# Kernel tuning notes

Hardware: AMD Instinct MI355X
Metric: run time of the kernel (lower is better)

Reference implementation:

```python
import jax, jax.numpy as jnp
import numpy as np

V, E, H, L, B, T = 8192, 64, 256, 2, 4, 512


def setup_inputs() -> dict:
    key = jax.random.key(0)
    ks = jax.random.split(key, 20)
    s = 0.02
    emb = (jax.random.normal(ks[0], (V, E)) * s).at[0].set(0.0)  # padding_idx=0
    x = jax.random.randint(ks[1], (B, T), 0, V)
    return {
        "x": x,
        "emb": emb,
        "W_ih0": jax.random.normal(ks[2], (H, E)) * s,
        "W_hh0": jax.random.normal(ks[3], (H, H)) * s,
        "b_ih0": jnp.zeros((H,), jnp.float32),
        "b_hh0": jnp.zeros((H,), jnp.float32),
        "W_ih1": jax.random.normal(ks[4], (H, H)) * s,
        "W_hh1": jax.random.normal(ks[5], (H, H)) * s,
        "b_ih1": jnp.zeros((H,), jnp.float32),
        "b_hh1": jnp.zeros((H,), jnp.float32),
        "Wq": jax.random.normal(ks[6], (H, H)) * s,
        "Wk": jax.random.normal(ks[7], (H, H)) * s,
        "v": jax.random.normal(ks[8], (H,)) * s,
        "gamma": jnp.ones((2 * H,), jnp.float32),
        "beta": jnp.zeros((2 * H,), jnp.float32),
        "Wfc": jax.random.normal(ks[9], (V, 2 * H)) * s,
        "bfc": jnp.zeros((V,), jnp.float32),
    }


def _rnn_layer(xs, W_ih, W_hh, b_ih, b_hh):
    # xs: (B, T, D) -> ys: (B, T, H), hT: (B, H). Vanilla tanh RNN.
    Bn = xs.shape[0]
    Hn = W_hh.shape[0]
    h0 = jnp.zeros((Bn, Hn), xs.dtype)

    def step(h, xt):
        h_new = jnp.tanh(xt @ W_ih.T + b_ih + h @ W_hh.T + b_hh)
        return h_new, h_new

    hT, ys = jax.lax.scan(step, h0, jnp.swapaxes(xs, 0, 1))
    return jnp.swapaxes(ys, 0, 1), hT


def reference(x, emb, W_ih0, W_hh0, b_ih0, b_hh0, W_ih1, W_hh1, b_ih1, b_hh1,
              Wq, Wk, v, gamma, beta, Wfc, bfc):
    # Dropout layers are identity (eval mode).
    e = emb[x]                                   # (B, T, E)
    y0, h0 = _rnn_layer(e, W_ih0, W_hh0, b_ih0, b_hh0)
    y1, h1 = _rnn_layer(y0, W_ih1, W_hh1, b_ih1, b_hh1)  # (B, T, H)

    # Bahdanau additive attention with causal mask
    q = y1 @ Wq.T                                # (B, T, H)
    k = y1 @ Wk.T                                # (B, T, H)
    # (B, Tq, Tk, H) broadcast add -> tanh -> contract with v
    scores = jnp.einsum('bijh,h->bij', jnp.tanh(q[:, :, None, :] + k[:, None, :, :]), v)
    Tn = scores.shape[1]
    causal = jnp.tril(jnp.ones((Tn, Tn), bool))
    scores = jnp.where(causal[None], scores, jnp.float32(-1e9))
    alpha = jax.nn.softmax(scores, axis=-1)      # (B, Tq, Tk)
    ctx = jnp.einsum('bij,bjh->bih', alpha, y1)  # bmm(alpha, K) with K = rnn_out

    cat = jnp.concatenate([y1, ctx], axis=-1)    # (B, T, 2H)
    mu = cat.mean(-1, keepdims=True)
    var = ((cat - mu) ** 2).mean(-1, keepdims=True)
    normed = (cat - mu) / jnp.sqrt(var + 1e-5) * gamma + beta

    logits = normed @ Wfc.T + bfc                # (B, T, V)
    h = jnp.stack([h0, h1], axis=0)              # (L, B, H)
    return logits, h
```

## Files before the change

kernel.cpp:

```cpp
#include <hip/hip_runtime.h>
#include <hip/hip_bf16.h>

typedef __bf16 bf16x8 __attribute__((ext_vector_type(8)));
typedef float  f32x4  __attribute__((ext_vector_type(4)));
typedef unsigned short u16;

#define T_N 512
#define H_N 256
#define B_N 4
#define V_N 8192
#define E_N 64

__device__ __forceinline__ float tanh_fast(float x) {
    float e = __expf(2.0f * x);
    return 1.0f - __fdividef(2.0f, e + 1.0f);
}

__device__ __forceinline__ u16 f2bf(float f) {
    __hip_bfloat16 h = __float2bfloat16(f);
    return __builtin_bit_cast(u16, h);
}

__device__ __forceinline__ bf16x8 as_bf16x8(uint4 u) {
    return __builtin_bit_cast(bf16x8, u);
}

__device__ __forceinline__ uint4 pack_bf8(f32x4 lo, f32x4 hi) {
    union { u16 s[8]; uint4 u; } r;
    #pragma unroll
    for (int e = 0; e < 4; ++e) { r.s[e] = f2bf(lo[e]); r.s[e+4] = f2bf(hi[e]); }
    return r.u;
}

__device__ __forceinline__ f32x4 mfma16(bf16x8 a, bf16x8 b, f32x4 c) {
    return __builtin_amdgcn_mfma_f32_16x16x32_bf16(a, b, c, 0, 0, 0);
}

__global__ void cvt_bf16_kernel(const float* __restrict__ src, u16* __restrict__ dst, int n4) {
    int i = blockIdx.x * 256 + threadIdx.x;
    if (i < n4) {
        f32x4 v = ((const f32x4*)src)[i];
        union { u16 s[4]; unsigned long long u; } r;
        #pragma unroll
        for (int e = 0; e < 4; ++e) r.s[e] = f2bf(v[e]);
        ((unsigned long long*)dst)[i] = r.u;
    }
}

__global__ __launch_bounds__(256)
void embed_xw0_kernel(const int* __restrict__ x, const float* __restrict__ emb,
                      const float* __restrict__ Wih, const float* __restrict__ bih,
                      const float* __restrict__ bhh, float* __restrict__ xw0) {
    const int t = blockIdx.x, tid = threadIdx.x;
    __shared__ float sE[4][64];
    {
        const int b = tid >> 6, k = tid & 63;
        sE[b][k] = emb[(size_t)x[b * T_N + t] * E_N + k];
    }
    __syncthreads();
    const int j = tid;
    const float* wr = Wih + j * E_N;
    float a0 = 0, a1 = 0, a2 = 0, a3 = 0;
    #pragma unroll 8
    for (int k = 0; k < E_N; ++k) {
        float wv = wr[k];
        a0 += sE[0][k] * wv; a1 += sE[1][k] * wv;
        a2 += sE[2][k] * wv; a3 += sE[3][k] * wv;
    }
    const float bs = bih[j] + bhh[j];
    f32x4 o = { a0 + bs, a1 + bs, a2 + bs, a3 + bs };
    *(f32x4*)(xw0 + ((size_t)t * H_N + j) * 4) = o;
}

template<int STORE_F32>
__global__ __launch_bounds__(256, 1)
void rnn_rec_kernel(const float* __restrict__ Whh, const float* __restrict__ xw,
                    u16* __restrict__ ybf, float* __restrict__ yf32,
                    float* __restrict__ hT) {
    __shared__ __align__(16) u16 hbuf[2][4][288];

    const int tid = threadIdx.x;
    const int w = tid >> 6, l = tid & 63;
    const int m = l & 15, g = l >> 4;
    const int b4 = m & 3;
    const int jmy = (w << 6) + l;

    for (int idx = tid; idx < 2 * 4 * 288; idx += 256) (&hbuf[0][0][0])[idx] = (u16)0;

    bf16x8 wfrag[4][8];
    #pragma unroll
    for (int nt = 0; nt < 4; ++nt) {
        const int j = (w << 6) + (nt << 4) + m;
        #pragma unroll
        for (int kk = 0; kk < 8; ++kk) {
            const float* p = Whh + (size_t)j * H_N + (kk << 5) + (g << 3);
            f32x4 lo = *(const f32x4*)p;
            f32x4 hi = *(const f32x4*)(p + 4);
            wfrag[nt][kk] = as_bf16x8(pack_bf8(lo, hi));
        }
    }

    const f32x4* xwv = (const f32x4*)xw;
    f32x4 xw_cur = xwv[jmy];
    __syncthreads();

    int cur = 0;
    for (int t = 0; t < T_N; ++t) {
        const int tn = (t + 1 < T_N) ? (t + 1) : t;
        f32x4 xw_nxt = xwv[(size_t)tn * H_N + jmy];

        bf16x8 af[8];
        #pragma unroll
        for (int kk = 0; kk < 8; ++kk)
            af[kk] = as_bf16x8(*(const uint4*)&hbuf[cur][b4][(kk << 5) + (g << 3)]);

        f32x4 ca[4], cb[4];
        #pragma unroll
        for (int nt = 0; nt < 4; ++nt) {
            ca[nt] = (f32x4){0.f, 0.f, 0.f, 0.f};
            cb[nt] = (f32x4){0.f, 0.f, 0.f, 0.f};
        }
        #pragma unroll
        for (int kk = 0; kk < 4; ++kk)
            #pragma unroll
            for (int nt = 0; nt < 4; ++nt) {
                ca[nt] = mfma16(af[kk],     wfrag[nt][kk],     ca[nt]);
                cb[nt] = mfma16(af[kk + 4], wfrag[nt][kk + 4], cb[nt]);
            }

        f32x4 hv = (g == 0) ? (ca[0] + cb[0])
                 : (g == 1) ? (ca[1] + cb[1])
                 : (g == 2) ? (ca[2] + cb[2])
                 :            (ca[3] + cb[3]);
        hv += xw_cur;

        #pragma unroll
        for (int b = 0; b < 4; ++b) {
            float hn = tanh_fast(hv[b]);
            u16 bits = f2bf(hn);
            hbuf[cur ^ 1][b][jmy] = bits;
            ybf[((size_t)b * T_N + t) * H_N + jmy] = bits;
            if (STORE_F32) yf32[((size_t)b * T_N + t) * H_N + jmy] = hn;
            if (t == T_N - 1) hT[b * H_N + jmy] = hn;
        }
        xw_cur = xw_nxt;
        cur ^= 1;

        asm volatile("s_waitcnt lgkmcnt(0)" ::: "memory");
        __builtin_amdgcn_s_barrier();
        __builtin_amdgcn_sched_barrier(0);
    }
}

template<int MODE>
__global__ __launch_bounds__(256, 2)
void gemm_bf16(const u16* __restrict__ A, const u16* __restrict__ Bw,
               float* __restrict__ out, const float* __restrict__ bias,
               const float* __restrict__ bias2, int M, int N, int K) {
    __shared__ __align__(16) u16 As[64][40];
    __shared__ __align__(16) u16 Bs[64][40];
    const int tid = threadIdx.x;
    const int nb = N >> 6;
    const int bm = blockIdx.x / nb, bn = blockIdx.x % nb;
    const int l = tid & 63, w = tid >> 6;
    const int wm = w & 1, wn = w >> 1;
    const int m = l & 15, g = l >> 4;
    const int srow = tid >> 2, sseg = tid & 3;

    f32x4 c[2][2];
    #pragma unroll
    for (int i = 0; i < 2; ++i)
        #pragma unroll
        for (int j = 0; j < 2; ++j) c[i][j] = (f32x4){0.f, 0.f, 0.f, 0.f};

    const u16* ap = A  + (size_t)(bm * 64 + srow) * K + sseg * 8;
    const u16* bp = Bw + (size_t)(bn * 64 + srow) * K + sseg * 8;

    for (int k0 = 0; k0 < K; k0 += 32) {
        uint4 av = *(const uint4*)(ap + k0);
        uint4 bv = *(const uint4*)(bp + k0);
        __syncthreads();
        *(uint4*)&As[srow][sseg << 3] = av;
        *(uint4*)&Bs[srow][sseg << 3] = bv;
        __syncthreads();
        bf16x8 af[2], bfr[2];
        #pragma unroll
        for (int i = 0; i < 2; ++i) {
            af[i]  = as_bf16x8(*(const uint4*)&As[(wm << 5) + (i << 4) + m][g << 3]);
            bfr[i] = as_bf16x8(*(const uint4*)&Bs[(wn << 5) + (i << 4) + m][g << 3]);
        }
        #pragma unroll
        for (int i = 0; i < 2; ++i)
            #pragma unroll
            for (int j = 0; j < 2; ++j)
                c[i][j] = mfma16(af[i], bfr[j], c[i][j]);
    }

    #pragma unroll
    for (int i = 0; i < 2; ++i)
        #pragma unroll
        for (int j = 0; j < 2; ++j) {
            const int col = (bn << 6) + (wn << 5) + (j << 4) + m;
            float bs = 0.f;
            if (bias)  bs += bias[col];
            if (bias2) bs += bias2[col];
            #pragma unroll
            for (int r = 0; r < 4; ++r) {
                const int row = (bm << 6) + (wm << 5) + (i << 4) + (g << 2) + r;
                const float val = c[i][j][r] + bs;
                if (MODE == 0) {
                    out[(size_t)row * N + col] = val;
                } else if (MODE == 1) {
                    const int b = row >> 9, t = row & 511;
                    out[((size_t)t * N + col) * 4 + b] = val;
                } else {
                    const int b = row >> 9, t = row & 511;
                    out[(size_t)b * N * T_N + (size_t)col * T_N + t] = val;
                }
            }
        }
}

__global__ __launch_bounds__(256, 2)
void gemm_fc(const u16* __restrict__ A, const u16* __restrict__ Bw,
             const float* __restrict__ bias, float* __restrict__ out) {
    __shared__ __align__(16) u16 As[128 * 32];
    __shared__ __align__(16) u16 Bs[128 * 32];
    const int tid = threadIdx.x;
    const int l = tid & 63, w = tid >> 6;
    const int m = l & 15, g = l >> 4;
    const int wm = w >> 1, wn = w & 1;
    const int bm = blockIdx.x >> 6, bn = blockIdx.x & 63;
    constexpr int K = 512;

    f32x4 acc[4][4];
    #pragma unroll
    for (int i = 0; i < 4; ++i)
        #pragma unroll
        for (int j = 0; j < 4; ++j) acc[i][j] = (f32x4){0.f, 0.f, 0.f, 0.f};

    const u16* aBase = A  + (size_t)(bm * 128) * K;
    const u16* bBase = Bw + (size_t)(bn * 128) * K;
    const int row0 = tid >> 2,          seg0 = tid & 3;
    const int row1 = (tid + 256) >> 2,  seg1 = tid & 3;
    const int wseg0 = seg0 ^ ((row0 >> 1) & 3);
    const int wseg1 = seg1 ^ ((row1 >> 1) & 3);

    for (int k0 = 0; k0 < K; k0 += 32) {
        uint4 av0 = *(const uint4*)(aBase + (size_t)row0 * K + k0 + seg0 * 8);
        uint4 av1 = *(const uint4*)(aBase + (size_t)row1 * K + k0 + seg1 * 8);
        uint4 bv0 = *(const uint4*)(bBase + (size_t)row0 * K + k0 + seg0 * 8);
        uint4 bv1 = *(const uint4*)(bBase + (size_t)row1 * K + k0 + seg1 * 8);
        __syncthreads();
        *(uint4*)((char*)As + row0 * 64 + wseg0 * 16) = av0;
        *(uint4*)((char*)As + row1 * 64 + wseg1 * 16) = av1;
        *(uint4*)((char*)Bs + row0 * 64 + wseg0 * 16) = bv0;
        *(uint4*)((char*)Bs + row1 * 64 + wseg1 * 16) = bv1;
        __syncthreads();
        bf16x8 af[4], bfr[4];
        #pragma unroll
        for (int i = 0; i < 4; ++i) {
            const int arow = wm * 64 + i * 16 + m;
            const int aslot = g ^ ((arow >> 1) & 3);
            af[i]  = as_bf16x8(*(const uint4*)((char*)As + arow * 64 + aslot * 16));
            const int brow = wn * 64 + i * 16 + m;
            const int bslot = g ^ ((brow >> 1) & 3);
            bfr[i] = as_bf16x8(*(const uint4*)((char*)Bs + brow * 64 + bslot * 16));
        }
        #pragma unroll
        for (int i = 0; i < 4; ++i)
            #pragma unroll
            for (int j = 0; j < 4; ++j)
                acc[i][j] = mfma16(af[i], bfr[j], acc[i][j]);
    }

    #pragma unroll
    for (int i = 0; i < 4; ++i)
        #pragma unroll
        for (int j = 0; j < 4; ++j) {
            const int col = bn * 128 + wn * 64 + j * 16 + m;
            const float bs = bias[col];
            #pragma unroll
            for (int r = 0; r < 4; ++r) {
                const int row = bm * 128 + wm * 64 + i * 16 + (g << 2) + r;
                out[(size_t)row * V_N + col] = acc[i][j][r] + bs;
            }
        }
}

__global__ __launch_bounds__(256)
void attn_kernel(const float* __restrict__ q, const float* __restrict__ kT,
                 const float* __restrict__ y1f, const float* __restrict__ vvec,
                 float* __restrict__ ctx) {
    const int blk = blockIdx.x;
    const int b = blk >> 9, i = blk & 511;
    const int tid = threadIdx.x;
    __shared__ float sQ[H_N], sV[H_N], sS[T_N];
    __shared__ float red[4];
    sQ[tid] = q[((size_t)b * T_N + i) * H_N + tid];
    sV[tid] = vvec[tid];
    __syncthreads();

    float s0 = -1e30f, s1 = -1e30f;
    if (tid <= i) {
        const float* kp = kT + (size_t)b * H_N * T_N + tid;
        float acc = 0.f;
        for (int h = 0; h < H_N; ++h) acc += sV[h] * tanh_fast(sQ[h] + kp[(size_t)h * T_N]);
        s0 = acc;
    }
    if (tid + 256 <= i) {
        const float* kp = kT + (size_t)b * H_N * T_N + tid + 256;
        float acc = 0.f;
        for (int h = 0; h < H_N; ++h) acc += sV[h] * tanh_fast(sQ[h] + kp[(size_t)h * T_N]);
        s1 = acc;
    }
    float mv = fmaxf(s0, s1);
    #pragma unroll
    for (int o = 32; o; o >>= 1) mv = fmaxf(mv, __shfl_xor(mv, o, 64));
    if ((tid & 63) == 0) red[tid >> 6] = mv;
    __syncthreads();
    mv = fmaxf(fmaxf(red[0], red[1]), fmaxf(red[2], red[3]));
    __syncthreads();
    float e0 = (tid <= i)       ? __expf(s0 - mv) : 0.f;
    float e1 = (tid + 256 <= i) ? __expf(s1 - mv) : 0.f;
    float sm = e0 + e1;
    #pragma unroll
    for (int o = 32; o; o >>= 1) sm += __shfl_xor(sm, o, 64);
    if ((tid & 63) == 0) red[tid >> 6] = sm;
    __syncthreads();
    sm = red[0] + red[1] + red[2] + red[3];
    const float rs = 1.0f / sm;
    sS[tid] = e0 * rs;
    sS[tid + 256] = e1 * rs;
    __syncthreads();
    float acc = 0.f;
    const float* yp = y1f + (size_t)b * T_N * H_N + tid;
    for (int j2 = 0; j2 <= i; ++j2) acc += sS[j2] * yp[(size_t)j2 * H_N];
    ctx[((size_t)b * T_N + i) * H_N + tid] = acc;
}

__global__ __launch_bounds__(256)
void ln_kernel(const float* __restrict__ y1f, const float* __restrict__ ctx,
               const float* __restrict__ gamma, const float* __restrict__ beta,
               u16* __restrict__ outbf) {
    const int row = blockIdx.x, tid = threadIdx.x;
    __shared__ float red[4];
    const float x1 = y1f[(size_t)row * H_N + tid];
    const float x2 = ctx[(size_t)row * H_N + tid];
    float s = x1 + x2;
    #pragma unroll
    for (int o = 32; o; o >>= 1) s += __shfl_xor(s, o, 64);
    if ((tid & 63) == 0) red[tid >> 6] = s;
    __syncthreads();
    const float mu = (red[0] + red[1] + red[2] + red[3]) * (1.f / 512.f);
    __syncthreads();
    const float d1 = x1 - mu, d2 = x2 - mu;
    float qv = d1 * d1 + d2 * d2;
    #pragma unroll
    for (int o = 32; o; o >>= 1) qv += __shfl_xor(qv, o, 64);
    if ((tid & 63) == 0) red[tid >> 6] = qv;
    __syncthreads();
    const float var = (red[0] + red[1] + red[2] + red[3]) * (1.f / 512.f);
    const float inv = rsqrtf(var + 1e-5f);
    outbf[(size_t)row * 512 + tid]       = f2bf(d1 * inv * gamma[tid] + beta[tid]);
    outbf[(size_t)row * 512 + tid + 256] = f2bf(d2 * inv * gamma[tid + 256] + beta[tid + 256]);
}

extern "C" void kernel_launch(void* const* d_in, const int* in_sizes, int n_in,
                              void* d_out, int out_size, void* d_ws, size_t ws_size,
                              hipStream_t stream) {
    const int*   x     = (const int*)  d_in[0];
    const float* emb   = (const float*)d_in[1];
    const float* Wih0  = (const float*)d_in[2];
    const float* Whh0  = (const float*)d_in[3];
    const float* bih0  = (const float*)d_in[4];
    const float* bhh0  = (const float*)d_in[5];
    const float* Wih1  = (const float*)d_in[6];
    const float* Whh1  = (const float*)d_in[7];
    const float* bih1  = (const float*)d_in[8];
    const float* bhh1  = (const float*)d_in[9];
    const float* Wq    = (const float*)d_in[10];
    const float* Wk    = (const float*)d_in[11];
    const float* vvec  = (const float*)d_in[12];
    const float* gamma = (const float*)d_in[13];
    const float* beta  = (const float*)d_in[14];
    const float* Wfc   = (const float*)d_in[15];
    const float* bfc   = (const float*)d_in[16];

    float* outp = (float*)d_out;
    char* ws = (char*)d_ws;
    float* xw0   = (float*)(ws + 0);
    float* xw1   = (float*)(ws + 2097152);
    u16*   y0bf  = (u16*)  (ws + 4194304);
    u16*   y1bf  = (u16*)  (ws + 5242880);
    float* y1f   = (float*)(ws + 6291456);
    float* qf    = (float*)(ws + 8388608);
    float* kT    = (float*)(ws + 10485760);
    float* ctx   = (float*)(ws + 12582912);
    u16*   nrm   = (u16*)  (ws + 14680064);
    u16*   Wih1b = (u16*)  (ws + 16777216);
    u16*   Wqb   = (u16*)  (ws + 16908288);
    u16*   Wkb   = (u16*)  (ws + 17039360);
    u16*   Wfcb  = (u16*)  (ws + 17170432);

    float* hout = outp + (size_t)B_N * T_N * V_N;

    cvt_bf16_kernel<<<64,   256, 0, stream>>>(Wih1, Wih1b, 65536 / 4);
    cvt_bf16_kernel<<<64,   256, 0, stream>>>(Wq,   Wqb,   65536 / 4);
    cvt_bf16_kernel<<<64,   256, 0, stream>>>(Wk,   Wkb,   65536 / 4);
    cvt_bf16_kernel<<<4096, 256, 0, stream>>>(Wfc,  Wfcb,  4194304 / 4);

    embed_xw0_kernel<<<512, 256, 0, stream>>>(x, emb, Wih0, bih0, bhh0, xw0);
    rnn_rec_kernel<0><<<1, 256, 0, stream>>>(Whh0, xw0, y0bf, nullptr, hout);
    gemm_bf16<1><<<32 * 4, 256, 0, stream>>>(y0bf, Wih1b, xw1, bih1, bhh1, 2048, 256, 256);
    rnn_rec_kernel<1><<<1, 256, 0, stream>>>(Whh1, xw1, y1bf, y1f, hout + 1024);
    gemm_bf16<0><<<32 * 4, 256, 0, stream>>>(y1bf, Wqb, qf, nullptr, nullptr, 2048, 256, 256);
    gemm_bf16<2><<<32 * 4, 256, 0, stream>>>(y1bf, Wkb, kT, nullptr, nullptr, 2048, 256, 256);
    attn_kernel<<<2048, 256, 0, stream>>>(qf, kT, y1f, vvec, ctx);
    ln_kernel<<<2048, 256, 0, stream>>>(y1f, ctx, gamma, beta, nrm);
    gemm_fc<<<16 * 64, 256, 0, stream>>>(nrm, Wfcb, bfc, outp);
}
```

Measured before the change: 1.023 ms.

## Fuse both RNN layers into one wavefront-pipelined kernel and use Pade tanh in attention

Replaces the two sequential single-block RNN kernels and the intermediate input-projection GEMM with one 512-thread kernel. Four waves run layer 0 at step t while four waves run layer 1 at step t-1, with W_ih1 held as bf16 in LDS and both hidden states exchanged through LDS. This removes one long serial recurrence, the y0 and xw1 round trips and a launch, at the cost of 128KB of LDS and more MFMA work per step on the layer-1 waves. The attention tanh is also swapped for a clamped Pade approximation to cut transcendental cost, with some extra accuracy risk.

After: 915.3 us. 10.5% less time.

```diff
diff --git a/kernel.cpp b/kernel.cpp
--- a/kernel.cpp
+++ b/kernel.cpp
@@ -14,6 +14,14 @@
 __device__ __forceinline__ float tanh_fast(float x) {
     float e = __expf(2.0f * x);
     return 1.0f - __fdividef(2.0f, e + 1.0f);
+}
+
+__device__ __forceinline__ float tanh_pade(float x) {
+    x = fminf(3.0f, fmaxf(-3.0f, x));
+    float x2 = x * x;
+    float num = x * (945.0f + x2 * (105.0f + x2));
+    float den = 945.0f + x2 * (420.0f + 15.0f * x2);
+    return num * __frcp_rn(den);
 }
 
 __device__ __forceinline__ u16 f2bf(float f) {
@@ -72,83 +80,142 @@
     *(f32x4*)(xw0 + ((size_t)t * H_N + j) * 4) = o;
 }
 
-template<int STORE_F32>
-__global__ __launch_bounds__(256, 1)
-void rnn_rec_kernel(const float* __restrict__ Whh, const float* __restrict__ xw,
-                    u16* __restrict__ ybf, float* __restrict__ yf32,
-                    float* __restrict__ hT) {
-    __shared__ __align__(16) u16 hbuf[2][4][288];
+__global__ __launch_bounds__(512, 2)
+void rnn_fused_kernel(const float* __restrict__ Whh0, const float* __restrict__ Wih1,
+                      const float* __restrict__ Whh1, const float* __restrict__ bih1,
+                      const float* __restrict__ bhh1, const float* __restrict__ xw0,
+                      u16* __restrict__ y1bf, float* __restrict__ y1f,
+                      float* __restrict__ hT) {
+    __shared__ __align__(16) u16 wih1_lds[128 * 512];
+    __shared__ __align__(16) u16 h0buf[2][4][288];
+    __shared__ __align__(16) u16 h1buf[2][4][288];
 
     const int tid = threadIdx.x;
     const int w = tid >> 6, l = tid & 63;
-    const int m = l & 15, g = l >> 4;
-    const int b4 = m & 3;
-    const int jmy = (w << 6) + l;
-
-    for (int idx = tid; idx < 2 * 4 * 288; idx += 256) (&hbuf[0][0][0])[idx] = (u16)0;
-
+    const int m = l & 15, g = l >> 4, b4 = m & 3;
+    const int layer = w >> 2, wl = w & 3;
+    const int jmy = (wl << 6) + l;
+
+    for (int idx = tid; idx < 2 * 4 * 288; idx += 512) {
+        (&h0buf[0][0][0])[idx] = (u16)0;
+        (&h1buf[0][0][0])[idx] = (u16)0;
+    }
+
+    for (int f = tid; f < 128 * 64; f += 512) {
+        const int grp = f >> 6, lo = f & 63;
+        const int jt = grp >> 3, kk = grp & 7;
+        const int mo = lo & 15, go = lo >> 4;
+        const float* p = Wih1 + (size_t)(jt * 16 + mo) * H_N + (kk << 5) + (go << 3);
+        f32x4 lo4 = *(const f32x4*)p;
+        f32x4 hi4 = *(const f32x4*)(p + 4);
+        *(uint4*)(wih1_lds + (size_t)f * 8) = pack_bf8(lo4, hi4);
+    }
+
+    const float* Whh = (layer == 0) ? Whh0 : Whh1;
     bf16x8 wfrag[4][8];
     #pragma unroll
     for (int nt = 0; nt < 4; ++nt) {
-        const int j = (w << 6) + (nt << 4) + m;
+        const int j = (wl << 6) + (nt << 4) + m;
         #pragma unroll
         for (int kk = 0; kk < 8; ++kk) {
             const float* p = Whh + (size_t)j * H_N + (kk << 5) + (g << 3);
-            f32x4 lo = *(const f32x4*)p;
-            f32x4 hi = *(const f32x4*)(p + 4);
-            wfrag[nt][kk] = as_bf16x8(pack_bf8(lo, hi));
-        }
-    }
-
-    const f32x4* xwv = (const f32x4*)xw;
+            f32x4 lo4 = *(const f32x4*)p;
+            f32x4 hi4 = *(const f32x4*)(p + 4);
+            wfrag[nt][kk] = as_bf16x8(pack_bf8(lo4, hi4));
+        }
+    }
+
+    const float bias1 = bih1[jmy] + bhh1[jmy];
+    const f32x4* xwv = (const f32x4*)xw0;
     f32x4 xw_cur = xwv[jmy];
-    __syncthreads();
-
-    int cur = 0;
-    for (int t = 0; t < T_N; ++t) {
-        const int tn = (t + 1 < T_N) ? (t + 1) : t;
-        f32x4 xw_nxt = xwv[(size_t)tn * H_N + jmy];
-
-        bf16x8 af[8];
-        #pragma unroll
-        for (int kk = 0; kk < 8; ++kk)
-            af[kk] = as_bf16x8(*(const uint4*)&hbuf[cur][b4][(kk << 5) + (g << 3)]);
-
-        f32x4 ca[4], cb[4];
-        #pragma unroll
-        for (int nt = 0; nt < 4; ++nt) {
-            ca[nt] = (f32x4){0.f, 0.f, 0.f, 0.f};
-            cb[nt] = (f32x4){0.f, 0.f, 0.f, 0.f};
-        }
-        #pragma unroll
-        for (int kk = 0; kk < 4; ++kk)
-            #pragma unroll
-            for (int nt = 0; nt < 4; ++nt) {
-                ca[nt] = mfma16(af[kk],     wfrag[nt][kk],     ca[nt]);
-                cb[nt] = mfma16(af[kk + 4], wfrag[nt][kk + 4], cb[nt]);
+
+    __syncthreads();
+
+    for (int it = 0; it < 513; ++it) {
+        const int rs = (it & 1) ^ 1;
+        if (layer == 0) {
+            if (it < 512) {
+                const int tn = (it + 1 < 512) ? it + 1 : it;
+                f32x4 xw_nxt = xwv[(size_t)tn * H_N + jmy];
+
+                bf16x8 af[8];
+                #pragma unroll
+                for (int kk = 0; kk < 8; ++kk)
+                    af[kk] = as_bf16x8(*(const uint4*)&h0buf[rs][b4][(kk << 5) + (g << 3)]);
+
+                f32x4 ca[4], cb[4];
+                #pragma unroll
+                for (int nt = 0; nt < 4; ++nt) {
+                    ca[nt] = (f32x4){0.f, 0.f, 0.f, 0.f};
+                    cb[nt] = (f32x4){0.f, 0.f, 0.f, 0.f};
+                }
+                #pragma unroll
+                for (int kk = 0; kk < 4; ++kk)
+                    #pragma unroll
+                    for (int nt = 0; nt < 4; ++nt) {
+                        ca[nt] = mfma16(af[kk],     wfrag[nt][kk],     ca[nt]);
+                        cb[nt] = mfma16(af[kk + 4], wfrag[nt][kk + 4], cb[nt]);
+                    }
+
+                f32x4 hv = (g == 0) ? (ca[0] + cb[0])
+                         : (g == 1) ? (ca[1] + cb[1])
+                         : (g == 2) ? (ca[2] + cb[2])
+                         :            (ca[3] + cb[3]);
+                hv += xw_cur;
+
+                #pragma unroll
+                for (int b = 0; b < 4; ++b) {
+                    float hn = tanh_fast(hv[b]);
+                    h0buf[it & 1][b][jmy] = f2bf(hn);
+                    if (it == T_N - 1) hT[b * H_N + jmy] = hn;
+                }
+                xw_cur = xw_nxt;
             }
-
-        f32x4 hv = (g == 0) ? (ca[0] + cb[0])
-                 : (g == 1) ? (ca[1] + cb[1])
-                 : (g == 2) ? (ca[2] + cb[2])
-                 :            (ca[3] + cb[3]);
-        hv += xw_cur;
-
-        #pragma unroll
-        for (int b = 0; b < 4; ++b) {
-            float hn = tanh_fast(hv[b]);
-            u16 bits = f2bf(hn);
-            hbuf[cur ^ 1][b][jmy] = bits;
-            ybf[((size_t)b * T_N + t) * H_N + jmy] = bits;
-            if (STORE_F32) yf32[((size_t)b * T_N + t) * H_N + jmy] = hn;
-            if (t == T_N - 1) hT[b * H_N + jmy] = hn;
-        }
-        xw_cur = xw_nxt;
-        cur ^= 1;
-
-        asm volatile("s_waitcnt lgkmcnt(0)" ::: "memory");
-        __builtin_amdgcn_s_barrier();
-        __builtin_amdgcn_sched_barrier(0);
+        } else {
+            if (it >= 1) {
+                const int s = it - 1;
+                f32x4 acc[2][4];
+                #pragma unroll
+                for (int hh = 0; hh < 2; ++hh)
+                    #pragma unroll
+                    for (int nt = 0; nt < 4; ++nt) acc[hh][nt] = (f32x4){0.f, 0.f, 0.f, 0.f};
+
+                #pragma unroll
+                for (int kk = 0; kk < 8; ++kk) {
+                    bf16x8 a0 = as_bf16x8(*(const uint4*)&h0buf[rs][b4][(kk << 5) + (g << 3)]);
+                    #pragma unroll
+                    for (int nt = 0; nt < 4; ++nt) {
+                        const int grp = ((wl << 2) + nt) * 8 + kk;
+                        bf16x8 bw = as_bf16x8(*(const uint4*)(wih1_lds + ((size_t)grp * 64 + l) * 8));
+                        acc[kk >> 2][nt] = mfma16(a0, bw, acc[kk >> 2][nt]);
+                    }
+                }
+                #pragma unroll
+                for (int kk = 0; kk < 8; ++kk) {
+                    bf16x8 a1 = as_bf16x8(*(const uint4*)&h1buf[rs][b4][(kk << 5) + (g << 3)]);
+                    #pragma unroll
+                    for (int nt = 0; nt < 4; ++nt)
+                        acc[kk >> 2][nt] = mfma16(a1, wfrag[nt][kk], acc[kk >> 2][nt]);
+                }
+
+                f32x4 hv = (g == 0) ? (acc[0][0] + acc[1][0])
+                         : (g == 1) ? (acc[0][1] + acc[1][1])
+                         : (g == 2) ? (acc[0][2] + acc[1][2])
+                         :            (acc[0][3] + acc[1][3]);
+                hv += (f32x4){bias1, bias1, bias1, bias1};
+
+                #pragma unroll
+                for (int b = 0; b < 4; ++b) {
+                    float hn = tanh_fast(hv[b]);
+                    u16 bits = f2bf(hn);
+                    h1buf[it & 1][b][jmy] = bits;
+                    y1bf[((size_t)b * T_N + s) * H_N + jmy] = bits;
+                    y1f [((size_t)b * T_N + s) * H_N + jmy] = hn;
+                    if (s == T_N - 1) hT[1024 + b * H_N + jmy] = hn;
+                }
+            }
+        }
+        asm volatile("s_waitcnt lgkmcnt(0)\n\ts_barrier" ::: "memory");
     }
 }
 
@@ -210,9 +277,6 @@
                 const float val = c[i][j][r] + bs;
                 if (MODE == 0) {
                     out[(size_t)row * N + col] = val;
-                } else if (MODE == 1) {
-                    const int b = row >> 9, t = row & 511;
-                    out[((size_t)t * N + col) * 4 + b] = val;
                 } else {
                     const int b = row >> 9, t = row & 511;
                     out[(size_t)b * N * T_N + (size_t)col * T_N + t] = val;
@@ -305,13 +369,13 @@
     if (tid <= i) {
         const float* kp = kT + (size_t)b * H_N * T_N + tid;
         float acc = 0.f;
-        for (int h = 0; h < H_N; ++h) acc += sV[h] * tanh_fast(sQ[h] + kp[(size_t)h * T_N]);
+        for (int h = 0; h < H_N; ++h) acc += sV[h] * tanh_pade(sQ[h] + kp[(size_t)h * T_N]);
         s0 = acc;
     }
     if (tid + 256 <= i) {
         const float* kp = kT + (size_t)b * H_N * T_N + tid + 256;
         float acc = 0.f;
-        for (int h = 0; h < H_N; ++h) acc += sV[h] * tanh_fast(sQ[h] + kp[(size_t)h * T_N]);
+        for (int h = 0; h < H_N; ++h) acc += sV[h] * tanh_pade(sQ[h] + kp[(size_t)h * T_N]);
         s1 = acc;
     }
     float mv = fmaxf(s0, s1);
@@ -390,30 +454,25 @@
     float* outp = (float*)d_out;
     char* ws = (char*)d_ws;
     float* xw0   = (float*)(ws + 0);
-    float* xw1   = (float*)(ws + 2097152);
-    u16*   y0bf  = (u16*)  (ws + 4194304);
     u16*   y1bf  = (u16*)  (ws + 5242880);
     float* y1f   = (float*)(ws + 6291456);
     float* qf    = (float*)(ws + 8388608);
     float* kT    = (float*)(ws + 10485760);
     float* ctx   = (float*)(ws + 12582912);
     u16*   nrm   = (u16*)  (ws + 14680064);
-    u16*   Wih1b = (u16*)  (ws + 16777216);
     u16*   Wqb   = (u16*)  (ws + 16908288);
     u16*   Wkb   = (u16*)  (ws + 17039360);
     u16*   Wfcb  = (u16*)  (ws + 17170432);
 
     float* hout = outp + (size_t)B_N * T_N * V_N;
 
-    cvt_bf16_kernel<<<64,   256, 0, stream>>>(Wih1, Wih1b, 65536 / 4);
-    cvt_bf16_kernel<<<64,   256, 0, stream>>>(Wq,   Wqb,   65536 / 4);
-    cvt_bf16_kernel<<<64,   256, 0, stream>>>(Wk,   Wkb,   65536 / 4);
-    cvt_bf16_kernel<<<4096, 256, 0, stream>>>(Wfc,  Wfcb,  4194304 / 4);
+    cvt_bf16_kernel<<<64,   256, 0, stream>>>(Wq,  Wqb,  65536 / 4);
+    cvt_bf16_kernel<<<64,   256, 0, stream>>>(Wk,  Wkb,  65536 / 4);
+    cvt_bf16_kernel<<<4096, 256, 0, stream>>>(Wfc, Wfcb, 4194304 / 4);
 
     embed_xw0_kernel<<<512, 256, 0, stream>>>(x, emb, Wih0, bih0, bhh0, xw0);
-    rnn_rec_kernel<0><<<1, 256, 0, stream>>>(Whh0, xw0, y0bf, nullptr, hout);
-    gemm_bf16<1><<<32 * 4, 256, 0, stream>>>(y0bf, Wih1b, xw1, bih1, bhh1, 2048, 256, 256);
-    rnn_rec_kernel<1><<<1, 256, 0, stream>>>(Whh1, xw1, y1bf, y1f, hout + 1024);
+    rnn_fused_kernel<<<1, 512, 0, stream>>>(Whh0, Wih1, Whh1, bih1, bhh1,
+                                            xw0, y1bf, y1f, hout);
     gemm_bf16<0><<<32 * 4, 256, 0, stream>>>(y1bf, Wqb, qf, nullptr, nullptr, 2048, 256, 256);
     gemm_bf16<2><<<32 * 4, 256, 0, stream>>>(y1bf, Wkb, kT, nullptr, nullptr, 2048, 256, 256);
     attn_kernel<<<2048, 256, 0, stream>>>(qf, kT, y1f, vvec, ctx);
```
